# Kernel tuning notes

Measured on AMD Instinct MI355X. Metric: run time of the kernel, lower is better.

The kernel has to match this reference:

```python
import jax, jax.numpy as jnp
import numpy as np
from jax import lax

# Static pair index table: all C(135,2)=9045 unordered node pairs (replaces the
# nested Python loops with a single gather).
PAIR_I, PAIR_J = np.triu_indices(135, k=1)
RRELU_SLOPE = (1.0 / 8.0 + 1.0 / 3.0) / 2.0  # eval-mode RReLU negative slope
BN_SCALE = 1.0 / float(np.sqrt(1.0 + 1e-5))  # eval BN with running mean=0, var=1


def _leaky(x):
    return jnp.where(x > 0, x, 0.01 * x)


def _conv1d(x, w, b):
    # x: (N, Cin, L), w: (Cout, Cin, K) -> (N, Cout, L-K+1), VALID
    y = lax.conv_general_dilated(x, w, (1,), 'VALID',
                                 dimension_numbers=('NCH', 'OIH', 'NCH'))
    return y + b[None, :, None]


def _bn_eval(x, g, b):
    # nn.BatchNorm1d in eval with fresh running stats (mean=0, var=1)
    return x * (g * BN_SCALE)[None, :, None] + b[None, :, None]


def _maxpool2d(x):
    # nn.MaxPool2d(2) applied to a 3D (N, H, W) tensor: 2x2 pool over (H, W)
    return lax.reduce_window(x, -jnp.inf, lax.max, (1, 2, 2), (1, 2, 2), 'VALID')


def setup_inputs() -> dict:
    key = jax.random.key(0)
    ks = iter(jax.random.split(key, 40))

    def w(shape, scale=0.05):
        return (jax.random.normal(next(ks), shape, jnp.float32) * scale)

    inp = {
        'x': jax.random.normal(next(ks), (30, 135, 375), jnp.float32),
        # FeatureExtractor
        'conv1_w': w((32, 1, 3)), 'conv1_b': jnp.zeros((32,), jnp.float32),
        'bn1_g': jnp.ones((32,), jnp.float32), 'bn1_b': jnp.zeros((32,), jnp.float32),
        'conv2_w': w((64, 16, 3)), 'conv2_b': jnp.zeros((64,), jnp.float32),
        'bn2_g': jnp.ones((64,), jnp.float32), 'bn2_b': jnp.zeros((64,), jnp.float32),
        'conv3_w': w((96, 32, 3)), 'conv3_b': jnp.zeros((96,), jnp.float32),
        'bn3_g': jnp.ones((96,), jnp.float32), 'bn3_b': jnp.zeros((96,), jnp.float32),
        'fe_fc_w': w((48 * 45, 32)), 'fe_fc_b': jnp.zeros((32,), jnp.float32),
        # SimilarityMeasureNetwork
        'sim_w1': w((64, 32)), 'sim_b1': jnp.zeros((32,), jnp.float32),
        'sim_w2': w((32, 16)), 'sim_b2': jnp.zeros((16,), jnp.float32),
        'sim_w3': w((16, 8)), 'sim_b3': jnp.zeros((8,), jnp.float32),
        'sim_w4': w((8, 1)), 'sim_b4': jnp.zeros((1,), jnp.float32),
        # ClassificationNet(9045, 3)
        'cls_w1': w((9045, 1024), 0.01), 'cls_b1': jnp.zeros((1024,), jnp.float32),
        'cls_w2': w((1024, 256)), 'cls_b2': jnp.zeros((256,), jnp.float32),
        'cls_w3': w((256, 64)), 'cls_b3': jnp.zeros((64,), jnp.float32),
        'cls_w4': w((64, 3)), 'cls_b4': jnp.zeros((3,), jnp.float32),
    }
    return inp


def reference(x, conv1_w, conv1_b, bn1_g, bn1_b, conv2_w, conv2_b, bn2_g, bn2_b,
              conv3_w, conv3_b, bn3_g, bn3_b, fe_fc_w, fe_fc_b,
              sim_w1, sim_b1, sim_w2, sim_b2, sim_w3, sim_b3, sim_w4, sim_b4,
              cls_w1, cls_b1, cls_w2, cls_b2, cls_w3, cls_b3, cls_w4, cls_b4):
    B = x.shape[0]  # 30 subjects
    h = x.reshape(B * 135, 1, 375)
    # FeatureExtractor (all subjects*nodes batched together)
    h = _maxpool2d(_leaky(_bn_eval(_conv1d(h, conv1_w, conv1_b), bn1_g, bn1_b)))  # (N,16,186)
    h = _maxpool2d(_leaky(_bn_eval(_conv1d(h, conv2_w, conv2_b), bn2_g, bn2_b)))  # (N,32,92)
    h = _maxpool2d(_leaky(_bn_eval(_conv1d(h, conv3_w, conv3_b), bn3_g, bn3_b)))  # (N,48,45)
    h = h.reshape(B * 135, -1) @ fe_fc_w + fe_fc_b  # (B*135, 32)
    feats = h.reshape(B, 135, 32)

    # All-pairs concat: single gather replacing the nested loops -> (B, 9045, 64)
    pi = jnp.asarray(PAIR_I)
    pj = jnp.asarray(PAIR_J)
    pairs = jnp.concatenate([feats[:, pi, :], feats[:, pj, :]], axis=-1)

    # SimilarityMeasureNetwork
    s = jax.nn.relu(pairs @ sim_w1 + sim_b1)
    s = jax.nn.relu(s @ sim_w2 + sim_b2)
    s = jax.nn.relu(s @ sim_w3 + sim_b3)
    s = jnp.tanh(s @ sim_w4 + sim_b4)  # (B, 9045, 1)
    subjects = s[..., 0]  # (B, 9045)

    # ClassificationNet (eval mode: RReLU -> fixed slope, dropout -> identity)
    c = subjects @ cls_w1 + cls_b1
    c = jnp.where(c >= 0, c, RRELU_SLOPE * c)
    c = jax.nn.relu(c @ cls_w2 + cls_b2)
    c = jax.nn.relu(c @ cls_w3 + cls_b3)
    c = c @ cls_w4 + cls_b4
    return jax.nn.log_softmax(c, axis=1)  # (B, 3)
```

## Files before the change

kernel.cpp:

```cpp
#include <hip/hip_runtime.h>
#include <math.h>

#define BN_SCALE 0.99999500003749967f
#define RRELU_SLOPE 0.22916666666666666f

static __device__ __forceinline__ float leaky(float v) { return v > 0.f ? v : 0.01f * v; }

typedef __attribute__((ext_vector_type(8))) short bf16x8;
typedef __attribute__((ext_vector_type(4))) float f32x4;

static __device__ __forceinline__ unsigned short f2bf(float f) {
  unsigned u = __builtin_bit_cast(unsigned, f);
  u = (u + 0x7FFFu + ((u >> 16) & 1u)) >> 16;
  return (unsigned short)u;
}

__global__ __launch_bounds__(256) void setup_kernel(
    const float* __restrict__ w2c, const float* __restrict__ g2,
    const float* __restrict__ w3c, const float* __restrict__ g3,
    const float* __restrict__ fcw, const float* __restrict__ fcb,
    const float* __restrict__ w1,  const float* __restrict__ b1,
    const float* __restrict__ cw1,
    unsigned short* __restrict__ w2frag,
    unsigned short* __restrict__ w3frag,
    unsigned short* __restrict__ bfragGG,
    float* __restrict__ bgagb,
    unsigned short* __restrict__ subjectsA,
    unsigned short* __restrict__ w1T)
{
  __shared__ float tile[64][65];
  const int t = threadIdx.x;
  if (blockIdx.x < 2272) {
    const int kt = blockIdx.x >> 4;
    const int ntb = blockIdx.x & 15;
    const int k0 = kt * 64, n0 = ntb * 64;
#pragma unroll 4
    for (int i = 0; i < 16; ++i) {
      const int idx = i * 256 + t;
      const int kk = idx >> 6, nn = idx & 63;
      const int k = k0 + kk;
      tile[kk][nn] = (k < 9045) ? cw1[(size_t)k * 1024 + n0 + nn] : 0.f;
    }
    __syncthreads();
#pragma unroll 4
    for (int i = 0; i < 8; ++i) {
      const int idx = i * 256 + t;
      const int nn = idx >> 5;
      const int kp = (idx & 31) * 2;
      const unsigned lo = f2bf(tile[kp][nn]);
      const unsigned hi = f2bf(tile[kp + 1][nn]);
      ((unsigned*)w1T)[(size_t)(n0 + nn) * 4544 + (k0 >> 1) + (idx & 31)] = lo | (hi << 16);
    }
    return;
  }
  const int item = (blockIdx.x - 2272) * 256 + t;
  if (item < 512) {
    const int tl = item >> 6, lane = item & 63;
    const int mt = tl >> 1, kc = tl & 1;
    const int lr = lane & 15, quad = lane >> 4;
    const int c = mt * 16 + lr;
    const float gs = g2[c] * BN_SCALE;
#pragma unroll
    for (int j = 0; j < 8; ++j) {
      const int k = quad * 8 + j;
      float v;
      if (kc == 0) { const int tap = k >> 4, ci = k & 15; v = w2c[c * 48 + ci * 3 + tap] * gs; }
      else         { v = (k < 16) ? w2c[c * 48 + k * 3 + 2] * gs : 0.f; }
      w2frag[item * 8 + j] = f2bf(v);
    }
  } else if (item < 1664) {
    const int it = item - 512;
    const int tl = it >> 6, lane = it & 63;
    const int mt = tl / 3, tap = tl - mt * 3;
    const int lr = lane & 15, quad = lane >> 4;
    const int c = mt * 16 + lr;
    const float gs = g3[c] * BN_SCALE;
#pragma unroll
    for (int j = 0; j < 8; ++j) {
      const int ci = quad * 8 + j;
      w3frag[it * 8 + j] = f2bf(w3c[c * 96 + ci * 3 + tap] * gs);
    }
  } else if (item < 19072) {
    const int it = item - 1664;
    const int chunk = it >> 8;
    const int rem = it & 255;
    const int nt = rem >> 6;
    const int lane = rem & 63;
    const int lr = lane & 15, quad = lane >> 4;
    const int n = nt * 16 + lr;
    const int off = (n >= 32) ? 32 : 0;
    const int nj = n & 31;
    float w1col[32];
#pragma unroll 8
    for (int q = 0; q < 32; ++q) w1col[q] = w1[(q + off) * 32 + nj];
#pragma unroll
    for (int j = 0; j < 8; ++j) {
      const int k = chunk * 32 + quad * 8 + j;
      float v = 0.f;
      if (k < 2160) {
        const float* fr = fcw + (size_t)k * 32;
#pragma unroll 8
        for (int q = 0; q < 32; ++q) v = fmaf(fr[q], w1col[q], v);
      }
      bfragGG[(size_t)it * 8 + j] = f2bf(v);
    }
  } else if (item < 19136) {
    const int n = item - 19072;
    const int off = (n >= 32) ? 32 : 0;
    const int nj = n & 31;
    float s = (n < 32) ? b1[nj] : 0.f;
    for (int q = 0; q < 32; ++q) s = fmaf(fcb[q], w1[(q + off) * 32 + nj], s);
    bgagb[n] = s;
  } else if (item < 55360) {
    const int idx = item - 19136;
    uint4 z = {0u, 0u, 0u, 0u};
    ((uint4*)subjectsA)[idx] = z;
  }
}

__global__ __launch_bounds__(128) void fe_kernel(
    const float* __restrict__ x,
    const float* __restrict__ w1c, const float* __restrict__ b1c,
    const float* __restrict__ g1,  const float* __restrict__ bb1,
    const float* __restrict__ b2c, const float* __restrict__ g2, const float* __restrict__ bb2,
    const float* __restrict__ b3c, const float* __restrict__ g3, const float* __restrict__ bb3,
    const unsigned short* __restrict__ w2frag,
    const unsigned short* __restrict__ w3frag,
    unsigned short* __restrict__ act3)
{
  __shared__ __align__(16) char smem[2 * 6912];
  const int t = threadIdx.x;
  const int wv = t >> 6, lane = t & 63, quad = lane >> 4, lr = lane & 15;
  const int n = blockIdx.x * 2 + wv;

  char* A = smem + wv * 6912;
  unsigned short* buf = (unsigned short*)A;
  float* be2 = (float*)(A + 6272);
  float* be3 = (float*)(A + 6528);

  bf16x8 a2[4][2];
#pragma unroll
  for (int mt = 0; mt < 4; ++mt)
#pragma unroll
    for (int kc = 0; kc < 2; ++kc)
      a2[mt][kc] = *(const bf16x8*)(w2frag + ((mt * 2 + kc) * 64 + lane) * 8);

  be2[lane] = b2c[lane] * (g2[lane] * BN_SCALE) + bb2[lane];
  be3[lane] = b3c[lane] * (g3[lane] * BN_SCALE) + bb3[lane];
  if (lane < 32) be3[64 + lane] = b3c[64 + lane] * (g3[64 + lane] * BN_SCALE) + bb3[64 + lane];
  ((unsigned*)buf)[1488 + lane] = 0;

  const int cp = lane & 7;
  float u[4][3], bbr[4];
#pragma unroll
  for (int d = 0; d < 4; ++d) {
    const int c = cp * 4 + d;
    const float gs = g1[c] * BN_SCALE;
    u[d][0] = w1c[c * 3 + 0] * gs;
    u[d][1] = w1c[c * 3 + 1] * gs;
    u[d][2] = w1c[c * 3 + 2] * gs;
    bbr[d] = b1c[c] * gs + bb1[c];
  }

  const float* xr = x + (size_t)n * 375;
  for (int o = lane; o < 1488; o += 64) {
    const int l = o >> 3;
    const int p = 2 * l;
    const float x0 = xr[p], x1 = xr[p + 1], x2 = xr[p + 2], x3 = xr[p + 3];
    unsigned pk = 0;
#pragma unroll
    for (int uu = 0; uu < 2; ++uu) {
      float m = -3.4e38f;
#pragma unroll
      for (int dc = 0; dc < 2; ++dc) {
        const int d = uu * 2 + dc;
        const float v0 = fmaf(x0, u[d][0], fmaf(x1, u[d][1], fmaf(x2, u[d][2], bbr[d])));
        const float v1 = fmaf(x1, u[d][0], fmaf(x2, u[d][1], fmaf(x3, u[d][2], bbr[d])));
        m = fmaxf(m, fmaxf(leaky(v0), leaky(v1)));
      }
      pk |= (unsigned)f2bf(m) << (16 * uu);
    }
    ((unsigned*)buf)[l * 8 + cp] = pk;
  }

  float be2r[4][4];
#pragma unroll
  for (int mt = 0; mt < 4; ++mt)
#pragma unroll
    for (int r = 0; r < 4; ++r) be2r[mt][r] = be2[mt * 16 + quad * 4 + r];

#pragma unroll 2
  for (int nt = 0; nt < 12; ++nt) {
    const int nrow = nt * 16 + lr;
    bf16x8 b0 = *(const bf16x8*)(buf + (nrow + (quad >> 1)) * 16 + (quad & 1) * 8);
    bf16x8 b1 = *(const bf16x8*)(buf + (nrow + 2) * 16 + (quad & 1) * 8);
    f32x4 acc[4];
#pragma unroll
    for (int mt = 0; mt < 4; ++mt)
#pragma unroll
      for (int r = 0; r < 4; ++r) acc[mt][r] = be2r[mt][r];
#pragma unroll
    for (int mt = 0; mt < 4; ++mt)
      acc[mt] = __builtin_amdgcn_mfma_f32_16x16x32_bf16(a2[mt][0], b0, acc[mt], 0, 0, 0);
#pragma unroll
    for (int mt = 0; mt < 4; ++mt)
      acc[mt] = __builtin_amdgcn_mfma_f32_16x16x32_bf16(a2[mt][1], b1, acc[mt], 0, 0, 0);
#pragma unroll
    for (int mt = 0; mt < 4; ++mt) {
      float o[4];
#pragma unroll
      for (int r = 0; r < 4; ++r) {
        const float v = leaky(acc[mt][r]);
        o[r] = fmaxf(v, __shfl_xor(v, 1));
      }
      if ((lr & 1) == 0) {
        const int np = nrow >> 1;
        if (np <= 91) {
          const float m0 = fmaxf(o[0], o[1]);
          const float m1 = fmaxf(o[2], o[3]);
          const unsigned pk = (unsigned)f2bf(m0) | ((unsigned)f2bf(m1) << 16);
          ((unsigned*)buf)[np * 16 + mt * 4 + quad] = pk;
        }
      }
    }
  }

  ((unsigned*)buf)[1472 + lane] = 0;
  if (lane < 32) ((unsigned*)buf)[1536 + lane] = 0;

  unsigned short* actr = act3 + (size_t)n * 2176;
  for (int mt = 0; mt < 6; ++mt) {
    bf16x8 a3[3];
#pragma unroll
    for (int tap = 0; tap < 3; ++tap)
      a3[tap] = *(const bf16x8*)(w3frag + ((mt * 3 + tap) * 64 + lane) * 8);
    float be3r[4];
#pragma unroll
    for (int r = 0; r < 4; ++r) be3r[r] = be3[mt * 16 + quad * 4 + r];
#pragma unroll
    for (int nt = 0; nt < 6; ++nt) {
      const int nrow = nt * 16 + lr;
      f32x4 acc;
#pragma unroll
      for (int r = 0; r < 4; ++r) acc[r] = be3r[r];
#pragma unroll
      for (int tap = 0; tap < 3; ++tap) {
        bf16x8 b = *(const bf16x8*)(buf + (nrow + tap) * 32 + quad * 8);
        acc = __builtin_amdgcn_mfma_f32_16x16x32_bf16(a3[tap], b, acc, 0, 0, 0);
      }
      float o[4];
#pragma unroll
      for (int r = 0; r < 4; ++r) {
        const float v = leaky(acc[r]);
        o[r] = fmaxf(v, __shfl_xor(v, 1));
      }
      if ((lr & 1) == 0) {
        const int np = nrow >> 1;
        if (np <= 44) {
          const int mp = mt * 8 + quad * 2;
          actr[mp * 45 + np] = f2bf(fmaxf(o[0], o[1]));
          actr[(mp + 1) * 45 + np] = f2bf(fmaxf(o[2], o[3]));
        }
      }
    }
  }
  if (lane < 16) actr[2160 + lane] = 0;
}

__global__ __launch_bounds__(256) void gagb_kernel(
    const unsigned short* __restrict__ act3,
    const unsigned short* __restrict__ bfragGG,
    const float* __restrict__ bgagb,
    float* __restrict__ Ga, float* __restrict__ Gb)
{
  __shared__ f32x4 sred[3][4][64];
  const int t = threadIdx.x;
  const int wv = t >> 6, lane = t & 63, quad = lane >> 4, lr = lane & 15;
  const int m0 = blockIdx.x * 16;
  const int arow = min(m0 + lr, 4049);

  f32x4 acc[4] = {};
  const int c0 = wv * 17;
  for (int chunk = c0; chunk < c0 + 17; ++chunk) {
    const bf16x8 a = *(const bf16x8*)(act3 + (size_t)arow * 2176 + chunk * 32 + quad * 8);
#pragma unroll
    for (int nt = 0; nt < 4; ++nt) {
      const bf16x8 b = *(const bf16x8*)(bfragGG + ((size_t)(chunk * 4 + nt) * 64 + lane) * 8);
      acc[nt] = __builtin_amdgcn_mfma_f32_16x16x32_bf16(a, b, acc[nt], 0, 0, 0);
    }
  }
  if (wv > 0) {
#pragma unroll
    for (int nt = 0; nt < 4; ++nt) sred[wv - 1][nt][lane] = acc[nt];
  }
  __syncthreads();
  if (wv == 0) {
#pragma unroll
    for (int nt = 0; nt < 4; ++nt) {
      f32x4 s = acc[nt];
#pragma unroll
      for (int q = 0; q < 3; ++q) {
        const f32x4 o = sred[q][nt][lane];
#pragma unroll
        for (int r = 0; r < 4; ++r) s[r] += o[r];
      }
      const int col = nt * 16 + lr;
      const float bias = bgagb[col];
#pragma unroll
      for (int r = 0; r < 4; ++r) {
        const int row = m0 + quad * 4 + r;
        if (row < 4050) {
          const float v = s[r] + bias;
          if (col < 32) Ga[row * 32 + col] = v;
          else          Gb[row * 32 + (col - 32)] = v;
        }
      }
    }
  }
}

__global__ __launch_bounds__(256) void sim_kernel(
    const float* __restrict__ Ga, const float* __restrict__ Gb,
    const float* __restrict__ w2, const float* __restrict__ b2,
    const float* __restrict__ w3, const float* __restrict__ b3,
    const float* __restrict__ w4, const float* __restrict__ b4,
    unsigned short* __restrict__ subjectsA)
{
  __shared__ float sGa[135 * 36];
  __shared__ float sGb[135 * 36];
  __shared__ float sw2[512], sw3[128], sw4[8];
  __shared__ float sb2[16], sb3[8], sb4v[1];

  const int t = threadIdx.x;
  const int b = blockIdx.x >> 5;
  const int c = blockIdx.x & 31;

  for (int i = t; i < 4320; i += 256) {
    const int r = i >> 5, col = i & 31;
    sGa[r * 36 + col] = Ga[b * 4320 + i];
    sGb[r * 36 + col] = Gb[b * 4320 + i];
  }
  for (int i = t; i < 512; i += 256) sw2[i] = w2[i];
  if (t < 128) sw3[t] = w3[t];
  if (t < 8) sw4[t] = w4[t];
  if (t < 16) sb2[t] = b2[t];
  if (t < 8) sb3[t] = b3[t];
  if (t == 0) sb4v[0] = b4[0];
  __syncthreads();

  const int mtile = b >> 4, lrm = b & 15;
  const int pend = min(9045, (c + 1) * 283);
  for (int p = c * 283 + t; p < pend; p += 256) {
    int i = (int)((269.0f - sqrtf((float)(72361 - 8 * p))) * 0.5f);
    i = max(0, min(133, i));
    while (134 * (i + 1) - ((i + 1) * i) / 2 <= p) ++i;
    while (134 * i - (i * (i - 1)) / 2 > p) --i;
    const int j = i + 1 + (p - (134 * i - (i * (i - 1)) / 2));

    float h1[32];
#pragma unroll
    for (int q = 0; q < 8; ++q) {
      const float4 va = *(const float4*)(&sGa[i * 36 + 4 * q]);
      const float4 vb = *(const float4*)(&sGb[j * 36 + 4 * q]);
      h1[4 * q + 0] = fmaxf(va.x + vb.x, 0.f);
      h1[4 * q + 1] = fmaxf(va.y + vb.y, 0.f);
      h1[4 * q + 2] = fmaxf(va.z + vb.z, 0.f);
      h1[4 * q + 3] = fmaxf(va.w + vb.w, 0.f);
    }

    float h2[16];
#pragma unroll
    for (int jj = 0; jj < 16; ++jj) h2[jj] = sb2[jj];
#pragma unroll 8
    for (int ii = 0; ii < 32; ++ii) {
      const float av = h1[ii];
      const float4* wr = reinterpret_cast<const float4*>(&sw2[ii * 16]);
#pragma unroll
      for (int r = 0; r < 4; ++r) {
        float4 w = wr[r];
        h2[4 * r + 0] = fmaf(av, w.x, h2[4 * r + 0]);
        h2[4 * r + 1] = fmaf(av, w.y, h2[4 * r + 1]);
        h2[4 * r + 2] = fmaf(av, w.z, h2[4 * r + 2]);
        h2[4 * r + 3] = fmaf(av, w.w, h2[4 * r + 3]);
      }
    }
#pragma unroll
    for (int jj = 0; jj < 16; ++jj) h2[jj] = fmaxf(h2[jj], 0.f);

    float h3[8];
#pragma unroll
    for (int jj = 0; jj < 8; ++jj) h3[jj] = sb3[jj];
#pragma unroll
    for (int ii = 0; ii < 16; ++ii) {
      const float av = h2[ii];
      const float4* wr = reinterpret_cast<const float4*>(&sw3[ii * 8]);
#pragma unroll
      for (int r = 0; r < 2; ++r) {
        float4 w = wr[r];
        h3[4 * r + 0] = fmaf(av, w.x, h3[4 * r + 0]);
        h3[4 * r + 1] = fmaf(av, w.y, h3[4 * r + 1]);
        h3[4 * r + 2] = fmaf(av, w.z, h3[4 * r + 2]);
        h3[4 * r + 3] = fmaf(av, w.w, h3[4 * r + 3]);
      }
    }
#pragma unroll
    for (int jj = 0; jj < 8; ++jj) h3[jj] = fmaxf(h3[jj], 0.f);

    float z = sb4v[0];
#pragma unroll
    for (int ii = 0; ii < 8; ++ii) z = fmaf(h3[ii], sw4[ii], z);

    const float az = fabsf(z);
    const float e = __expf(-2.f * az);
    const float rr = (1.f - e) / (1.f + e);
    const float val = copysignf(rr, z);

    const int chunk = p >> 5, q8 = (p & 31) >> 3, jj2 = p & 7;
    subjectsA[chunk * 1024 + mtile * 512 + (q8 * 16 + lrm) * 8 + jj2] = f2bf(val);
  }
}

__global__ __launch_bounds__(256) void c1_kernel(
    const unsigned short* __restrict__ subjectsA,
    const unsigned short* __restrict__ w1T,
    float* __restrict__ part)
{
  const int t = threadIdx.x;
  const int wv = t >> 6, lane = t & 63, quad = lane >> 4, lr = lane & 15;
  const int job = blockIdx.x * 4 + wv;
  const int ng = job & 15;
  const int kg = job >> 4;
  const int c0 = kg * 5;
  const int cend = min(283, c0 + 5);

  f32x4 acc[2][4] = {};
  for (int ch = c0; ch < cend; ++ch) {
    const bf16x8 a0 = *(const bf16x8*)(subjectsA + ch * 1024 + lane * 8);
    const bf16x8 a1 = *(const bf16x8*)(subjectsA + ch * 1024 + 512 + lane * 8);
#pragma unroll
    for (int nt = 0; nt < 4; ++nt) {
      const int col = (ng * 4 + nt) * 16 + lr;
      const bf16x8 b = *(const bf16x8*)(w1T + (size_t)col * 9088 + ch * 32 + quad * 8);
      acc[0][nt] = __builtin_amdgcn_mfma_f32_16x16x32_bf16(a0, b, acc[0][nt], 0, 0, 0);
      acc[1][nt] = __builtin_amdgcn_mfma_f32_16x16x32_bf16(a1, b, acc[1][nt], 0, 0, 0);
    }
  }
#pragma unroll
  for (int mt = 0; mt < 2; ++mt)
#pragma unroll
    for (int r = 0; r < 4; ++r) {
      const int m = mt * 16 + quad * 4 + r;
      if (m < 30) {
#pragma unroll
        for (int nt = 0; nt < 4; ++nt) {
          const int col = (ng * 4 + nt) * 16 + lr;
          part[(size_t)(m * 64 + kg) * 1024 + col] = acc[mt][nt][r];
        }
      }
    }
}

__global__ __launch_bounds__(256) void tail_a_kernel(
    const float* __restrict__ part,
    const float* __restrict__ cb1,
    float* __restrict__ act1)
{
  const int r = blockIdx.x >> 2;
  const int cg = blockIdx.x & 3;
  const int j = cg * 256 + threadIdx.x;
  float s = cb1[j];
  const float* pp = part + (size_t)r * 64 * 1024 + j;
#pragma unroll 8
  for (int q = 0; q < 64; ++q) s += pp[q * 1024];
  act1[r * 1024 + j] = s >= 0.f ? s : RRELU_SLOPE * s;
}

__global__ __launch_bounds__(256) void tail_b_kernel(
    const float* __restrict__ act1,
    const float* __restrict__ w2, const float* __restrict__ cb2,
    float* __restrict__ act2)
{
  __shared__ float sa[1024];
  __shared__ float sp[256];
  const int r = blockIdx.x >> 3;
  const int cg = blockIdx.x & 7;
  const int t = threadIdx.x;
  const int c = t & 31;
  const int ks = t >> 5;
  const int col = cg * 32 + c;

  for (int i = t; i < 1024; i += 256) sa[i] = act1[r * 1024 + i];
  __syncthreads();

  float acc = 0.f;
  const int k0 = ks * 128;
  for (int kk = k0; kk < k0 + 128; kk += 4) {
    const float4 a = *reinterpret_cast<const float4*>(&sa[kk]);
    acc = fmaf(a.x, w2[(kk + 0) * 256 + col], acc);
    acc = fmaf(a.y, w2[(kk + 1) * 256 + col], acc);
    acc = fmaf(a.z, w2[(kk + 2) * 256 + col], acc);
    acc = fmaf(a.w, w2[(kk + 3) * 256 + col], acc);
  }
  sp[t] = acc;
  __syncthreads();
  if (t < 32) {
    float s = cb2[col];
#pragma unroll
    for (int q = 0; q < 8; ++q) s += sp[q * 32 + t];
    act2[r * 256 + cg * 32 + t] = fmaxf(s, 0.f);
  }
}

__global__ __launch_bounds__(256) void tail_c_kernel(
    const float* __restrict__ act2,
    const float* __restrict__ w3, const float* __restrict__ cb3,
    const float* __restrict__ w4, const float* __restrict__ cb4,
    float* __restrict__ out)
{
  __shared__ float sa[256];
  __shared__ float sp[256];
  __shared__ float sc3[64];
  __shared__ float slg[3];
  const int r = blockIdx.x, t = threadIdx.x;
  const int c = t & 63;
  const int ks = t >> 6;

  sa[t] = act2[r * 256 + t];
  __syncthreads();
  {
    float acc = 0.f;
    const int k0 = ks * 64;
#pragma unroll 4
    for (int kk = k0; kk < k0 + 64; ++kk)
      acc = fmaf(sa[kk], w3[kk * 64 + c], acc);
    sp[t] = acc;
  }
  __syncthreads();
  if (t < 64) {
    const float s = cb3[t] + sp[t] + sp[t + 64] + sp[t + 128] + sp[t + 192];
    sc3[t] = fmaxf(s, 0.f);
  }
  __syncthreads();
  if (t < 3) {
    float acc = cb4[t];
#pragma unroll
    for (int kk = 0; kk < 64; ++kk) acc = fmaf(sc3[kk], w4[kk * 3 + t], acc);
    slg[t] = acc;
  }
  __syncthreads();
  if (t == 0) {
    float m = fmaxf(slg[0], fmaxf(slg[1], slg[2]));
    float se = __expf(slg[0] - m) + __expf(slg[1] - m) + __expf(slg[2] - m);
    float lse = m + logf(se);
    out[r * 3 + 0] = slg[0] - lse;
    out[r * 3 + 1] = slg[1] - lse;
    out[r * 3 + 2] = slg[2] - lse;
  }
}

extern "C" void kernel_launch(void* const* d_in, const int* in_sizes, int n_in,
                              void* d_out, int out_size, void* d_ws, size_t ws_size,
                              hipStream_t stream) {
  const float* x    = (const float*)d_in[0];
  const float* w1c  = (const float*)d_in[1];
  const float* b1c  = (const float*)d_in[2];
  const float* g1   = (const float*)d_in[3];
  const float* bb1  = (const float*)d_in[4];
  const float* w2c  = (const float*)d_in[5];
  const float* b2c  = (const float*)d_in[6];
  const float* g2   = (const float*)d_in[7];
  const float* bb2  = (const float*)d_in[8];
  const float* w3c  = (const float*)d_in[9];
  const float* b3c  = (const float*)d_in[10];
  const float* g3   = (const float*)d_in[11];
  const float* bb3  = (const float*)d_in[12];
  const float* fcw  = (const float*)d_in[13];
  const float* fcb  = (const float*)d_in[14];
  const float* sw1  = (const float*)d_in[15];
  const float* sb1  = (const float*)d_in[16];
  const float* sw2  = (const float*)d_in[17];
  const float* sb2  = (const float*)d_in[18];
  const float* sw3  = (const float*)d_in[19];
  const float* sb3  = (const float*)d_in[20];
  const float* sw4  = (const float*)d_in[21];
  const float* sb4  = (const float*)d_in[22];
  const float* cw1  = (const float*)d_in[23];
  const float* cb1  = (const float*)d_in[24];
  const float* cw2  = (const float*)d_in[25];
  const float* cb2  = (const float*)d_in[26];
  const float* cw3  = (const float*)d_in[27];
  const float* cb3  = (const float*)d_in[28];
  const float* cw4  = (const float*)d_in[29];
  const float* cb4  = (const float*)d_in[30];

  float* ws = (float*)d_ws;
  float* Ga    = ws;
  float* Gb    = ws + 129600;
  float* part  = ws + 259200;
  float* bgagb = ws + 2225280;
  float* act1  = ws + 2225344;
  float* act2  = ws + 2256064;
  unsigned short* wsu = (unsigned short*)(ws + 2263744);
  unsigned short* w2frag    = wsu;
  unsigned short* w3frag    = wsu + 4096;
  unsigned short* bfragGG   = wsu + 13312;
  unsigned short* act3      = wsu + 152576;
  unsigned short* subjectsA = wsu + 8965376;
  unsigned short* w1T       = wsu + 9255168;

  setup_kernel<<<2489, 256, 0, stream>>>(w2c, g2, w3c, g3, fcw, fcb, sw1, sb1, cw1,
                                         w2frag, w3frag, bfragGG, bgagb, subjectsA, w1T);
  fe_kernel<<<2025, 128, 0, stream>>>(x, w1c, b1c, g1, bb1, b2c, g2, bb2,
                                      b3c, g3, bb3, w2frag, w3frag, act3);
  gagb_kernel<<<254, 256, 0, stream>>>(act3, bfragGG, bgagb, Ga, Gb);
  sim_kernel<<<960, 256, 0, stream>>>(Ga, Gb, sw2, sb2, sw3, sb3, sw4, sb4, subjectsA);
  c1_kernel<<<256, 256, 0, stream>>>(subjectsA, w1T, part);
  tail_a_kernel<<<120, 256, 0, stream>>>(part, cb1, act1);
  tail_b_kernel<<<240, 256, 0, stream>>>(act1, cw2, cb2, act2);
  tail_c_kernel<<<30, 256, 0, stream>>>(act2, cw3, cb3, cw4, cb4, (float*)d_out);
}
```

Measured before the change: 263.5 us.

## Split each feature-extractor sample across two waves and apply leaky after pooling

The fe_kernel now assigns one sample per 128-thread block instead of one sample per wave. The two waves split conv1 elements, conv2 N-tiles and conv3 M-tiles, and __syncthreads separates the stages. Layer outputs go to separate shared buffers, so conv3 no longer overwrites the conv1 data in place. Leaky ReLU is now applied once after the max-pool rather than on every element before it, which is valid because leaky is monotonic. This cuts per-wave serial work and some ALU operations, at the cost of block barriers and twice as many blocks.

```diff
diff --git a/kernel.cpp b/kernel.cpp
--- a/kernel.cpp
+++ b/kernel.cpp
@@ -128,15 +128,14 @@
     const unsigned short* __restrict__ w3frag,
     unsigned short* __restrict__ act3)
 {
-  __shared__ __align__(16) char smem[2 * 6912];
+  __shared__ __align__(16) unsigned short s1t[194 * 16];
+  __shared__ __align__(16) unsigned short s2t[98 * 32];
+  __shared__ float be2[64];
+  __shared__ float be3[96];
+
   const int t = threadIdx.x;
   const int wv = t >> 6, lane = t & 63, quad = lane >> 4, lr = lane & 15;
-  const int n = blockIdx.x * 2 + wv;
-
-  char* A = smem + wv * 6912;
-  unsigned short* buf = (unsigned short*)A;
-  float* be2 = (float*)(A + 6272);
-  float* be3 = (float*)(A + 6528);
+  const int n = blockIdx.x;
 
   bf16x8 a2[4][2];
 #pragma unroll
@@ -145,10 +144,10 @@
     for (int kc = 0; kc < 2; ++kc)
       a2[mt][kc] = *(const bf16x8*)(w2frag + ((mt * 2 + kc) * 64 + lane) * 8);
 
-  be2[lane] = b2c[lane] * (g2[lane] * BN_SCALE) + bb2[lane];
-  be3[lane] = b3c[lane] * (g3[lane] * BN_SCALE) + bb3[lane];
-  if (lane < 32) be3[64 + lane] = b3c[64 + lane] * (g3[64 + lane] * BN_SCALE) + bb3[64 + lane];
-  ((unsigned*)buf)[1488 + lane] = 0;
+  if (t < 64) be2[t] = b2c[t] * (g2[t] * BN_SCALE) + bb2[t];
+  if (t < 96) be3[t] = b3c[t] * (g3[t] * BN_SCALE) + bb3[t];
+  if (t < 64) ((unsigned*)s1t)[1488 + t] = 0;
+  if (t < 96) ((unsigned*)s2t)[1472 + t] = 0;
 
   const int cp = lane & 7;
   float u[4][3], bbr[4];
@@ -163,7 +162,7 @@
   }
 
   const float* xr = x + (size_t)n * 375;
-  for (int o = lane; o < 1488; o += 64) {
+  for (int o = t; o < 1488; o += 128) {
     const int l = o >> 3;
     const int p = 2 * l;
     const float x0 = xr[p], x1 = xr[p + 1], x2 = xr[p + 2], x3 = xr[p + 3];
@@ -176,12 +175,13 @@
         const int d = uu * 2 + dc;
         const float v0 = fmaf(x0, u[d][0], fmaf(x1, u[d][1], fmaf(x2, u[d][2], bbr[d])));
         const float v1 = fmaf(x1, u[d][0], fmaf(x2, u[d][1], fmaf(x3, u[d][2], bbr[d])));
-        m = fmaxf(m, fmaxf(leaky(v0), leaky(v1)));
-      }
-      pk |= (unsigned)f2bf(m) << (16 * uu);
-    }
-    ((unsigned*)buf)[l * 8 + cp] = pk;
-  }
+        m = fmaxf(m, fmaxf(v0, v1));
+      }
+      pk |= (unsigned)f2bf(leaky(m)) << (16 * uu);
+    }
+    ((unsigned*)s1t)[l * 8 + cp] = pk;
+  }
+  __syncthreads();
 
   float be2r[4][4];
 #pragma unroll
@@ -190,10 +190,11 @@
     for (int r = 0; r < 4; ++r) be2r[mt][r] = be2[mt * 16 + quad * 4 + r];
 
 #pragma unroll 2
-  for (int nt = 0; nt < 12; ++nt) {
+  for (int nti = 0; nti < 6; ++nti) {
+    const int nt = wv * 6 + nti;
     const int nrow = nt * 16 + lr;
-    bf16x8 b0 = *(const bf16x8*)(buf + (nrow + (quad >> 1)) * 16 + (quad & 1) * 8);
-    bf16x8 b1 = *(const bf16x8*)(buf + (nrow + 2) * 16 + (quad & 1) * 8);
+    bf16x8 b0 = *(const bf16x8*)(s1t + (nrow + (quad >> 1)) * 16 + (quad & 1) * 8);
+    bf16x8 b1 = *(const bf16x8*)(s1t + (nrow + 2) * 16 + (quad & 1) * 8);
     f32x4 acc[4];
 #pragma unroll
     for (int mt = 0; mt < 4; ++mt)
@@ -209,27 +210,24 @@
     for (int mt = 0; mt < 4; ++mt) {
       float o[4];
 #pragma unroll
-      for (int r = 0; r < 4; ++r) {
-        const float v = leaky(acc[mt][r]);
-        o[r] = fmaxf(v, __shfl_xor(v, 1));
-      }
+      for (int r = 0; r < 4; ++r)
+        o[r] = fmaxf(acc[mt][r], __shfl_xor(acc[mt][r], 1));
       if ((lr & 1) == 0) {
         const int np = nrow >> 1;
         if (np <= 91) {
-          const float m0 = fmaxf(o[0], o[1]);
-          const float m1 = fmaxf(o[2], o[3]);
+          const float m0 = leaky(fmaxf(o[0], o[1]));
+          const float m1 = leaky(fmaxf(o[2], o[3]));
           const unsigned pk = (unsigned)f2bf(m0) | ((unsigned)f2bf(m1) << 16);
-          ((unsigned*)buf)[np * 16 + mt * 4 + quad] = pk;
+          ((unsigned*)s2t)[np * 16 + mt * 4 + quad] = pk;
         }
       }
     }
   }
-
-  ((unsigned*)buf)[1472 + lane] = 0;
-  if (lane < 32) ((unsigned*)buf)[1536 + lane] = 0;
+  __syncthreads();
 
   unsigned short* actr = act3 + (size_t)n * 2176;
-  for (int mt = 0; mt < 6; ++mt) {
+  for (int mti = 0; mti < 3; ++mti) {
+    const int mt = wv * 3 + mti;
     bf16x8 a3[3];
 #pragma unroll
     for (int tap = 0; tap < 3; ++tap)
@@ -245,26 +243,24 @@
       for (int r = 0; r < 4; ++r) acc[r] = be3r[r];
 #pragma unroll
       for (int tap = 0; tap < 3; ++tap) {
-        bf16x8 b = *(const bf16x8*)(buf + (nrow + tap) * 32 + quad * 8);
+        bf16x8 b = *(const bf16x8*)(s2t + (nrow + tap) * 32 + quad * 8);
         acc = __builtin_amdgcn_mfma_f32_16x16x32_bf16(a3[tap], b, acc, 0, 0, 0);
       }
       float o[4];
 #pragma unroll
-      for (int r = 0; r < 4; ++r) {
-        const float v = leaky(acc[r]);
-        o[r] = fmaxf(v, __shfl_xor(v, 1));
-      }
+      for (int r = 0; r < 4; ++r)
+        o[r] = fmaxf(acc[r], __shfl_xor(acc[r], 1));
       if ((lr & 1) == 0) {
         const int np = nrow >> 1;
         if (np <= 44) {
           const int mp = mt * 8 + quad * 2;
-          actr[mp * 45 + np] = f2bf(fmaxf(o[0], o[1]));
-          actr[(mp + 1) * 45 + np] = f2bf(fmaxf(o[2], o[3]));
+          actr[mp * 45 + np] = f2bf(leaky(fmaxf(o[0], o[1])));
+          actr[(mp + 1) * 45 + np] = f2bf(leaky(fmaxf(o[2], o[3])));
         }
       }
     }
   }
-  if (lane < 16) actr[2160 + lane] = 0;
+  if (t < 16) actr[2160 + t] = 0;
 }
 
 __global__ __launch_bounds__(256) void gagb_kernel(
@@ -610,7 +606,7 @@
 
   setup_kernel<<<2489, 256, 0, stream>>>(w2c, g2, w3c, g3, fcw, fcb, sw1, sb1, cw1,
                                          w2frag, w3frag, bfragGG, bgagb, subjectsA, w1T);
-  fe_kernel<<<2025, 128, 0, stream>>>(x, w1c, b1c, g1, bb1, b2c, g2, bb2,
+  fe_kernel<<<4050, 128, 0, stream>>>(x, w1c, b1c, g1, bb1, b2c, g2, bb2,
                                       b3c, g3, bb3, w2frag, w3frag, act3);
   gagb_kernel<<<254, 256, 0, stream>>>(act3, bfragGG, bgagb, Ga, Gb);
   sim_kernel<<<960, 256, 0, stream>>>(Ga, Gb, sw2, sb2, sw3, sb3, sw4, sb4, subjectsA);
```

After: 261.9 us. Within noise of the previous version (-0.6%).

## Stream fp32 classifier weights directly instead of per-call bf16 transpose

Applied to the files above, without the earlier changes.

Drops the per-call transpose and bf16 conversion of the 9045x1024 classifier weight in the setup kernel, along with zeroing the padded subjects buffer. The first classifier layer becomes a scalar fp32 FMA kernel that reads cw1 once in row-major order, with subjects stored transposed in fp32, and reduces two k-halves through shared memory. This removes one full read and write pass over the large weight each call, at the cost of giving up MFMA for that GEMM. It also applies leaky ReLU after the max-pool instead of before, which is valid because leaky ReLU is monotonic, and saves a few ALU ops.

```diff
diff --git a/kernel.cpp b/kernel.cpp
--- a/kernel.cpp
+++ b/kernel.cpp
@@ -20,40 +20,12 @@
     const float* __restrict__ w3c, const float* __restrict__ g3,
     const float* __restrict__ fcw, const float* __restrict__ fcb,
     const float* __restrict__ w1,  const float* __restrict__ b1,
-    const float* __restrict__ cw1,
     unsigned short* __restrict__ w2frag,
     unsigned short* __restrict__ w3frag,
     unsigned short* __restrict__ bfragGG,
-    float* __restrict__ bgagb,
-    unsigned short* __restrict__ subjectsA,
-    unsigned short* __restrict__ w1T)
-{
-  __shared__ float tile[64][65];
-  const int t = threadIdx.x;
-  if (blockIdx.x < 2272) {
-    const int kt = blockIdx.x >> 4;
-    const int ntb = blockIdx.x & 15;
-    const int k0 = kt * 64, n0 = ntb * 64;
-#pragma unroll 4
-    for (int i = 0; i < 16; ++i) {
-      const int idx = i * 256 + t;
-      const int kk = idx >> 6, nn = idx & 63;
-      const int k = k0 + kk;
-      tile[kk][nn] = (k < 9045) ? cw1[(size_t)k * 1024 + n0 + nn] : 0.f;
-    }
-    __syncthreads();
-#pragma unroll 4
-    for (int i = 0; i < 8; ++i) {
-      const int idx = i * 256 + t;
-      const int nn = idx >> 5;
-      const int kp = (idx & 31) * 2;
-      const unsigned lo = f2bf(tile[kp][nn]);
-      const unsigned hi = f2bf(tile[kp + 1][nn]);
-      ((unsigned*)w1T)[(size_t)(n0 + nn) * 4544 + (k0 >> 1) + (idx & 31)] = lo | (hi << 16);
-    }
-    return;
-  }
-  const int item = (blockIdx.x - 2272) * 256 + t;
+    float* __restrict__ bgagb)
+{
+  const int item = blockIdx.x * 256 + threadIdx.x;
   if (item < 512) {
     const int tl = item >> 6, lane = item & 63;
     const int mt = tl >> 1, kc = tl & 1;
@@ -111,10 +83,6 @@
     float s = (n < 32) ? b1[nj] : 0.f;
     for (int q = 0; q < 32; ++q) s = fmaf(fcb[q], w1[(q + off) * 32 + nj], s);
     bgagb[n] = s;
-  } else if (item < 55360) {
-    const int idx = item - 19136;
-    uint4 z = {0u, 0u, 0u, 0u};
-    ((uint4*)subjectsA)[idx] = z;
   }
 }
 
@@ -176,9 +144,9 @@
         const int d = uu * 2 + dc;
         const float v0 = fmaf(x0, u[d][0], fmaf(x1, u[d][1], fmaf(x2, u[d][2], bbr[d])));
         const float v1 = fmaf(x1, u[d][0], fmaf(x2, u[d][1], fmaf(x3, u[d][2], bbr[d])));
-        m = fmaxf(m, fmaxf(leaky(v0), leaky(v1)));
-      }
-      pk |= (unsigned)f2bf(m) << (16 * uu);
+        m = fmaxf(m, fmaxf(v0, v1));
+      }
+      pk |= (unsigned)f2bf(leaky(m)) << (16 * uu);
     }
     ((unsigned*)buf)[l * 8 + cp] = pk;
   }
@@ -209,15 +177,13 @@
     for (int mt = 0; mt < 4; ++mt) {
       float o[4];
 #pragma unroll
-      for (int r = 0; r < 4; ++r) {
-        const float v = leaky(acc[mt][r]);
-        o[r] = fmaxf(v, __shfl_xor(v, 1));
-      }
+      for (int r = 0; r < 4; ++r)
+        o[r] = fmaxf(acc[mt][r], __shfl_xor(acc[mt][r], 1));
       if ((lr & 1) == 0) {
         const int np = nrow >> 1;
         if (np <= 91) {
-          const float m0 = fmaxf(o[0], o[1]);
-          const float m1 = fmaxf(o[2], o[3]);
+          const float m0 = leaky(fmaxf(o[0], o[1]));
+          const float m1 = leaky(fmaxf(o[2], o[3]));
           const unsigned pk = (unsigned)f2bf(m0) | ((unsigned)f2bf(m1) << 16);
           ((unsigned*)buf)[np * 16 + mt * 4 + quad] = pk;
         }
@@ -250,16 +216,14 @@
       }
       float o[4];
 #pragma unroll
-      for (int r = 0; r < 4; ++r) {
-        const float v = leaky(acc[r]);
-        o[r] = fmaxf(v, __shfl_xor(v, 1));
-      }
+      for (int r = 0; r < 4; ++r)
+        o[r] = fmaxf(acc[r], __shfl_xor(acc[r], 1));
       if ((lr & 1) == 0) {
         const int np = nrow >> 1;
         if (np <= 44) {
           const int mp = mt * 8 + quad * 2;
-          actr[mp * 45 + np] = f2bf(fmaxf(o[0], o[1]));
-          actr[(mp + 1) * 45 + np] = f2bf(fmaxf(o[2], o[3]));
+          actr[mp * 45 + np] = f2bf(leaky(fmaxf(o[0], o[1])));
+          actr[(mp + 1) * 45 + np] = f2bf(leaky(fmaxf(o[2], o[3])));
         }
       }
     }
@@ -324,7 +288,7 @@
     const float* __restrict__ w2, const float* __restrict__ b2,
     const float* __restrict__ w3, const float* __restrict__ b3,
     const float* __restrict__ w4, const float* __restrict__ b4,
-    unsigned short* __restrict__ subjectsA)
+    float* __restrict__ subjectsT)
 {
   __shared__ float sGa[135 * 36];
   __shared__ float sGb[135 * 36];
@@ -348,7 +312,6 @@
   if (t == 0) sb4v[0] = b4[0];
   __syncthreads();
 
-  const int mtile = b >> 4, lrm = b & 15;
   const int pend = min(9045, (c + 1) * 283);
   for (int p = c * 283 + t; p < pend; p += 256) {
     int i = (int)((269.0f - sqrtf((float)(72361 - 8 * p))) * 0.5f);
@@ -415,49 +378,68 @@
     const float rr = (1.f - e) / (1.f + e);
     const float val = copysignf(rr, z);
 
-    const int chunk = p >> 5, q8 = (p & 31) >> 3, jj2 = p & 7;
-    subjectsA[chunk * 1024 + mtile * 512 + (q8 * 16 + lrm) * 8 + jj2] = f2bf(val);
+    subjectsT[(size_t)p * 32 + b] = val;
   }
 }
 
 __global__ __launch_bounds__(256) void c1_kernel(
-    const unsigned short* __restrict__ subjectsA,
-    const unsigned short* __restrict__ w1T,
+    const float* __restrict__ subjectsT,
+    const float* __restrict__ cw1,
     float* __restrict__ part)
 {
+  __shared__ float sred[128 * 30];
   const int t = threadIdx.x;
-  const int wv = t >> 6, lane = t & 63, quad = lane >> 4, lr = lane & 15;
-  const int job = blockIdx.x * 4 + wv;
-  const int ng = job & 15;
-  const int kg = job >> 4;
-  const int c0 = kg * 5;
-  const int cend = min(283, c0 + 5);
-
-  f32x4 acc[2][4] = {};
-  for (int ch = c0; ch < cend; ++ch) {
-    const bf16x8 a0 = *(const bf16x8*)(subjectsA + ch * 1024 + lane * 8);
-    const bf16x8 a1 = *(const bf16x8*)(subjectsA + ch * 1024 + 512 + lane * 8);
-#pragma unroll
-    for (int nt = 0; nt < 4; ++nt) {
-      const int col = (ng * 4 + nt) * 16 + lr;
-      const bf16x8 b = *(const bf16x8*)(w1T + (size_t)col * 9088 + ch * 32 + quad * 8);
-      acc[0][nt] = __builtin_amdgcn_mfma_f32_16x16x32_bf16(a0, b, acc[0][nt], 0, 0, 0);
-      acc[1][nt] = __builtin_amdgcn_mfma_f32_16x16x32_bf16(a1, b, acc[1][nt], 0, 0, 0);
-    }
-  }
-#pragma unroll
-  for (int mt = 0; mt < 2; ++mt)
-#pragma unroll
-    for (int r = 0; r < 4; ++r) {
-      const int m = mt * 16 + quad * 4 + r;
-      if (m < 30) {
-#pragma unroll
-        for (int nt = 0; nt < 4; ++nt) {
-          const int col = (ng * 4 + nt) * 16 + lr;
-          part[(size_t)(m * 64 + kg) * 1024 + col] = acc[mt][nt][r];
-        }
-      }
-    }
+  const int cg = blockIdx.x & 7;
+  const int kg = blockIdx.x >> 3;
+  const int col = cg * 128 + (t & 127);
+  const int ksub = t >> 7;
+  const int k0 = kg * 142 + ksub * 71;
+  const int kend = min(9045, k0 + 71);
+
+  float acc[30];
+#pragma unroll
+  for (int m = 0; m < 30; ++m) acc[m] = 0.f;
+
+  for (int k = k0; k < kend; ++k) {
+    const float w = cw1[(size_t)k * 1024 + col];
+    const float* sr = subjectsT + (size_t)k * 32;
+    const float4 s0 = *(const float4*)(sr + 0);
+    const float4 s1 = *(const float4*)(sr + 4);
+    const float4 s2 = *(const float4*)(sr + 8);
+    const float4 s3 = *(const float4*)(sr + 12);
+    const float4 s4 = *(const float4*)(sr + 16);
+    const float4 s5 = *(const float4*)(sr + 20);
+    const float4 s6 = *(const float4*)(sr + 24);
+    const float2 s7 = *(const float2*)(sr + 28);
+    acc[0]  = fmaf(s0.x, w, acc[0]);  acc[1]  = fmaf(s0.y, w, acc[1]);
+    acc[2]  = fmaf(s0.z, w, acc[2]);  acc[3]  = fmaf(s0.w, w, acc[3]);
+    acc[4]  = fmaf(s1.x, w, acc[4]);  acc[5]  = fmaf(s1.y, w, acc[5]);
+    acc[6]  = fmaf(s1.z, w, acc[6]);  acc[7]  = fmaf(s1.w, w, acc[7]);
+    acc[8]  = fmaf(s2.x, w, acc[8]);  acc[9]  = fmaf(s2.y, w, acc[9]);
+    acc[10] = fmaf(s2.z, w, acc[10]); acc[11] = fmaf(s2.w, w, acc[11]);
+    acc[12] = fmaf(s3.x, w, acc[12]); acc[13] = fmaf(s3.y, w, acc[13]);
+    acc[14] = fmaf(s3.z, w, acc[14]); acc[15] = fmaf(s3.w, w, acc[15]);
+    acc[16] = fmaf(s4.x, w, acc[16]); acc[17] = fmaf(s4.y, w, acc[17]);
+    acc[18] = fmaf(s4.z, w, acc[18]); acc[19] = fmaf(s4.w, w, acc[19]);
+    acc[20] = fmaf(s5.x, w, acc[20]); acc[21] = fmaf(s5.y, w, acc[21]);
+    acc[22] = fmaf(s5.z, w, acc[22]); acc[23] = fmaf(s5.w, w, acc[23]);
+    acc[24] = fmaf(s6.x, w, acc[24]); acc[25] = fmaf(s6.y, w, acc[25]);
+    acc[26] = fmaf(s6.z, w, acc[26]); acc[27] = fmaf(s6.w, w, acc[27]);
+    acc[28] = fmaf(s7.x, w, acc[28]); acc[29] = fmaf(s7.y, w, acc[29]);
+  }
+
+  if (ksub == 1) {
+#pragma unroll
+    for (int m = 0; m < 30; ++m) sred[(t - 128) * 30 + m] = acc[m];
+  }
+  __syncthreads();
+  if (ksub == 0) {
+#pragma unroll
+    for (int m = 0; m < 30; ++m) {
+      const float v = acc[m] + sred[t * 30 + m];
+      part[(size_t)(m * 64 + kg) * 1024 + col] = v;
+    }
+  }
 }
 
 __global__ __launch_bounds__(256) void tail_a_kernel(
@@ -600,21 +582,20 @@
   float* bgagb = ws + 2225280;
   float* act1  = ws + 2225344;
   float* act2  = ws + 2256064;
-  unsigned short* wsu = (unsigned short*)(ws + 2263744);
+  float* subjectsT = ws + 2263744;
+  unsigned short* wsu = (unsigned short*)(ws + 2553184);
   unsigned short* w2frag    = wsu;
   unsigned short* w3frag    = wsu + 4096;
   unsigned short* bfragGG   = wsu + 13312;
   unsigned short* act3      = wsu + 152576;
-  unsigned short* subjectsA = wsu + 8965376;
-  unsigned short* w1T       = wsu + 9255168;
-
-  setup_kernel<<<2489, 256, 0, stream>>>(w2c, g2, w3c, g3, fcw, fcb, sw1, sb1, cw1,
-                                         w2frag, w3frag, bfragGG, bgagb, subjectsA, w1T);
+
+  setup_kernel<<<75, 256, 0, stream>>>(w2c, g2, w3c, g3, fcw, fcb, sw1, sb1,
+                                       w2frag, w3frag, bfragGG, bgagb);
   fe_kernel<<<2025, 128, 0, stream>>>(x, w1c, b1c, g1, bb1, b2c, g2, bb2,
                                       b3c, g3, bb3, w2frag, w3frag, act3);
   gagb_kernel<<<254, 256, 0, stream>>>(act3, bfragGG, bgagb, Ga, Gb);
-  sim_kernel<<<960, 256, 0, stream>>>(Ga, Gb, sw2, sb2, sw3, sb3, sw4, sb4, subjectsA);
-  c1_kernel<<<256, 256, 0, stream>>>(subjectsA, w1T, part);
+  sim_kernel<<<960, 256, 0, stream>>>(Ga, Gb, sw2, sb2, sw3, sb3, sw4, sb4, subjectsT);
+  c1_kernel<<<512, 256, 0, stream>>>(subjectsT, cw1, part);
   tail_a_kernel<<<120, 256, 0, stream>>>(part, cb1, act1);
   tail_b_kernel<<<240, 256, 0, stream>>>(act1, cw2, cb2, act2);
   tail_c_kernel<<<30, 256, 0, stream>>>(act2, cw3, cb3, cw4, cb4, (float*)d_out);
```

After: 295.4 us. 1.12x slower.
